# Performance work log

Measured on AMD Instinct MI355X. Metric: run time of the kernel, lower is better.

Reference implementation:

```python
import jax, jax.numpy as jnp
import numpy as np

B, S, E, NH = 2, 1024, 2048, 16
DH = E // NH
EPS = 1e-6

def setup_inputs() -> dict:
    key = jax.random.key(0)
    ks = jax.random.split(key, 6)
    q = jax.random.normal(ks[0], (B, S, E), dtype=jnp.float32)
    k = jax.random.normal(ks[1], (B, S, E), dtype=jnp.float32)
    v = jax.random.normal(ks[2], (B, S, E), dtype=jnp.float32)
    Wi = jax.random.normal(ks[3], (3 * E, NH), dtype=jnp.float32) * 0.02
    bi = jax.random.normal(ks[4], (NH,), dtype=jnp.float32) * 0.1
    Wf = jax.random.normal(ks[5], (3 * E, NH), dtype=jnp.float32) * 0.02
    bf = jnp.linspace(3.0, 6.0, NH, dtype=jnp.float32)  # bias_linspace_initializer(3,6)
    ln_scale = jnp.ones((E,), dtype=jnp.float32)
    return {"q": q, "k": k, "v": v, "Wi": Wi, "bi": bi, "Wf": Wf, "bf": bf, "ln_scale": ln_scale}

def _mlstm_forward(q, k, v, Wi, bi, Wf, bf, ln_scale):
    b, s, e = q.shape
    nh = Wi.shape[1]
    dh = e // nh
    x = jnp.concatenate([q, k, v], axis=-1)                     # (B,S,3E)
    ig = (x @ Wi + bi).transpose(0, 2, 1)[..., None]            # (B,NH,S,1)
    fg = (x @ Wf + bf).transpose(0, 2, 1)[..., None]            # (B,NH,S,1)
    split = lambda t: t.reshape(b, s, nh, dh).transpose(0, 2, 1, 3)
    qh, kh, vh = split(q), split(k), split(v)                   # (B,NH,S,DH)
    # parallel_stabilized_simple backend
    log_f = jax.nn.log_sigmoid(fg)                              # (B,NH,S,1)
    log_f_cum = jnp.concatenate(
        [jnp.zeros((b, nh, 1, 1), q.dtype), jnp.cumsum(log_f, axis=2)], axis=2
    )                                                           # (B,NH,S+1,1)
    # D[i,j] = cumsum[i] - cumsum[j] on causal part
    fg_mat = log_f_cum - jnp.transpose(log_f_cum, (0, 1, 3, 2)) # (B,NH,S+1,S+1)
    ltr = jnp.tril(jnp.ones((s, s), dtype=bool))
    log_fg = jnp.where(ltr, fg_mat[:, :, 1:, 1:], -jnp.inf)     # (B,NH,S,S)
    log_D = log_fg + jnp.transpose(ig, (0, 1, 3, 2))            # + i_j per column
    max_log_D = jnp.max(log_D, axis=-1, keepdims=True)          # (B,NH,S,1)
    D = jnp.exp(log_D - max_log_D)
    qk = jnp.einsum('bhsd,bhtd->bhst', qh, kh) / jnp.sqrt(jnp.asarray(dh, q.dtype))
    C = qk * D                                                  # (B,NH,S,S)
    normalizer = jnp.maximum(jnp.abs(C.sum(-1, keepdims=True)), jnp.exp(-max_log_D))
    Cn = C / (normalizer + EPS)
    h = jnp.einsum('bhst,bhtd->bhsd', Cn, vh)                   # (B,NH,S,DH)
    # MultiHeadLayerNorm: normalize over DH per head, scale (no bias)
    mu = h.mean(-1, keepdims=True)
    var = ((h - mu) ** 2).mean(-1, keepdims=True)
    hn = (h - mu) * jax.lax.rsqrt(var + EPS)
    hn = hn * ln_scale.reshape(1, nh, 1, dh)
    return hn.transpose(0, 2, 1, 3).reshape(b, s, e)            # (B,S,E)

def reference(q, k, v, Wi, bi, Wf, bf, ln_scale):
    return _mlstm_forward(q, k, v, Wi, bi, Wf, bf, ln_scale)
```

## Files before the change

### kernel.cpp

```cpp
#include <hip/hip_runtime.h>
#include <hip/hip_bf16.h>

#define B_   2
#define S_   1024
#define E_   2048
#define NH_  16
#define DH_  128
#define EPS_ 1e-6f

using half8   = __attribute__((ext_vector_type(8))) _Float16;
using floatx4 = __attribute__((ext_vector_type(4))) float;

__device__ __forceinline__ half8 cvt8h(const float* __restrict__ p) {
    float4 a = *(const float4*)p;
    float4 b = *(const float4*)(p + 4);
    half8 r;
    r[0] = (_Float16)a.x; r[1] = (_Float16)a.y;
    r[2] = (_Float16)a.z; r[3] = (_Float16)a.w;
    r[4] = (_Float16)b.x; r[5] = (_Float16)b.y;
    r[6] = (_Float16)b.z; r[7] = (_Float16)b.w;
    return r;
}

__global__ __launch_bounds__(256, 4) void gates_kernel(
    const float* __restrict__ q, const float* __restrict__ k,
    const float* __restrict__ v, const float* __restrict__ Wi,
    const float* __restrict__ Wf, float* __restrict__ pre_i,
    float* __restrict__ pre_f, _Float16* __restrict__ qhg,
    _Float16* __restrict__ khg, _Float16* __restrict__ vtg)
{
    __shared__ __attribute__((aligned(16))) _Float16 xs[32 * 264];
    __shared__ __attribute__((aligned(16))) _Float16 wt[32 * 264];

    const int t    = threadIdx.x;
    const int w    = t >> 6, lane = t & 63, quad = lane >> 4, l15 = lane & 15;
    const int mw   = w & 1, nw = w >> 1;
    const int m0   = blockIdx.x * 32;
    const int by   = blockIdx.y;
    const int kbase = by * 768;
    const int bblk = m0 >> 10;
    const int s0   = m0 & 1023;

    floatx4 acc = {0.f, 0.f, 0.f, 0.f};

    for (int c = 0; c < 3; ++c) {
        __syncthreads();
        const int e0   = kbase + c * 256;
        const int tsel = e0 >> 11;
        const int el0  = e0 & 2047;
        const float* xb = (tsel == 0) ? q : (tsel == 1) ? k : v;
        _Float16* fout = (tsel == 0) ? qhg : khg;
        #pragma unroll
        for (int i = 0; i < 4; ++i) {
            int g = t + i * 256;
            int row = g >> 5, grp = g & 31;
            half8 s8 = cvt8h(xb + (size_t)(m0 + row) * E_ + el0 + grp * 8);
            *(half8*)(&xs[row * 264 + grp * 8]) = s8;
            if (tsel < 2) {
                int el = el0 + grp * 8;
                int h  = el >> 7, d = el & 127;
                *(half8*)(fout + ((size_t)(bblk * NH_ + h) * S_ + s0 + row) * DH_ + d) = s8;
            }
        }
        {
            const int kk = t;
            const float* wiRow = Wi + (size_t)(e0 + kk) * NH_;
            const float* wfRow = Wf + (size_t)(e0 + kk) * NH_;
            float wif[16], wff[16];
            #pragma unroll
            for (int i4 = 0; i4 < 4; ++i4) {
                float4 a = *(const float4*)(wiRow + i4 * 4);
                wif[i4*4+0]=a.x; wif[i4*4+1]=a.y; wif[i4*4+2]=a.z; wif[i4*4+3]=a.w;
                float4 b = *(const float4*)(wfRow + i4 * 4);
                wff[i4*4+0]=b.x; wff[i4*4+1]=b.y; wff[i4*4+2]=b.z; wff[i4*4+3]=b.w;
            }
            #pragma unroll
            for (int hh = 0; hh < 16; ++hh) wt[hh * 264 + kk]        = (_Float16)wif[hh];
            #pragma unroll
            for (int hh = 0; hh < 16; ++hh) wt[(16 + hh) * 264 + kk] = (_Float16)wff[hh];
        }
        __syncthreads();
        if (tsel == 2) {
            const int col = t;
            const int el  = el0 + col;
            const int h   = el >> 7, d = el & 127;
            _Float16 tmp[32];
            #pragma unroll
            for (int r = 0; r < 32; ++r) tmp[r] = xs[r * 264 + col];
            const size_t vo = ((size_t)(bblk * NH_ + h) * DH_ + d) * S_ + s0;
            #pragma unroll
            for (int i = 0; i < 4; ++i)
                *(half8*)(vtg + vo + i * 8) = *(half8*)(&tmp[i * 8]);
        }
        #pragma unroll
        for (int ks = 0; ks < 8; ++ks) {
            half8 af = *(const half8*)(&xs[(mw * 16 + l15) * 264 + ks * 32 + quad * 8]);
            half8 bw = *(const half8*)(&wt[(nw * 16 + l15) * 264 + ks * 32 + quad * 8]);
            acc = __builtin_amdgcn_mfma_f32_16x16x32_f16(af, bw, acc, 0, 0, 0);
        }
    }
    #pragma unroll
    for (int reg = 0; reg < 4; ++reg) {
        int m   = m0 + mw * 16 + quad * 4 + reg;
        int b   = m >> 10, s = m & 1023;
        int col = nw * 16 + l15;
        float vacc = acc[reg];
        if (col < 16)
            pre_i[((size_t)(by * 32 + b * NH_ + col)) * S_ + s] = vacc;
        else
            pre_f[((size_t)(by * 32 + b * NH_ + col - 16)) * S_ + s] = vacc;
    }
}

__global__ __launch_bounds__(256, 2) void attn_kernel(
    const _Float16* __restrict__ qh, const _Float16* __restrict__ kh,
    const _Float16* __restrict__ vtg, const float* __restrict__ pre_i,
    const float* __restrict__ pre_f, const float* __restrict__ bi,
    const float* __restrict__ bfb, const float* __restrict__ lnsc,
    float* __restrict__ out)
{
    __shared__ __attribute__((aligned(16))) _Float16 Ks[64 * 136];
    __shared__ __attribute__((aligned(16))) _Float16 Vt[128 * 72];
    __shared__ __attribute__((aligned(16))) _Float16 Pb[64 * 72];
    __shared__ __attribute__((aligned(16))) float ajAll[1024];
    __shared__ float cq64[64], nf64[64];
    __shared__ float wsum[4], wmax[4];
    __shared__ float lpart[2][2][32];
    __shared__ float spart[2][2][32];
    __shared__ float qpart[2][2][32];

    const int t    = threadIdx.x;
    const int w    = t >> 6, lane = t & 63, quad = lane >> 4, l15 = lane & 15;
    const int mw   = w & 1, nw = w >> 1;
    const int L    = blockIdx.x;
    int qi, bh;
    if (L < 256) { qi = L >> 5;                bh = L & 31; }
    else         { qi = 15 - ((L - 256) >> 5); bh = (L - 256) & 31; }
    const int b    = bh >> 4, h = bh & 15;
    const int q0   = qi * 64;
    const int krow = t >> 2, kd0 = (t & 3) * 32;
    const int vd   = t >> 1, vj0 = (t & 1) * 32;

    {
        const int e4 = t * 4;
        const float bih = bi[h], bfh = bfb[h];
        float ig4[4] = {bih, bih, bih, bih};
        float x4[4]  = {bfh, bfh, bfh, bfh};
        #pragma unroll
        for (int y = 0; y < 8; ++y) {
            float4 pi = *(const float4*)(pre_i + ((size_t)(y * 32 + bh)) * S_ + e4);
            float4 pf = *(const float4*)(pre_f + ((size_t)(y * 32 + bh)) * S_ + e4);
            ig4[0] += pi.x; ig4[1] += pi.y; ig4[2] += pi.z; ig4[3] += pi.w;
            x4[0]  += pf.x; x4[1]  += pf.y; x4[2]  += pf.z; x4[3]  += pf.w;
        }
        float lf[4], ls = 0.f;
        #pragma unroll
        for (int e = 0; e < 4; ++e) {
            float x = x4[e];
            float l = (x >= 0.f) ? -log1pf(__expf(-x)) : (x - log1pf(__expf(x)));
            ls += l; lf[e] = ls;
        }
        float sc = ls;
        #pragma unroll
        for (int off = 1; off < 64; off <<= 1) {
            float o = __shfl_up(sc, off);
            if (lane >= off) sc += o;
        }
        float sexcl = sc - ls;
        if (lane == 63) wsum[w] = sc;
        __syncthreads();
        float Foff = 0.f;
        for (int i = 0; i < w; ++i) Foff += wsum[i];
        float Fbase = Foff + sexcl;
        float av[4], lm[4], am = -3.0e38f;
        #pragma unroll
        for (int e = 0; e < 4; ++e) {
            float F = Fbase + lf[e];
            float a = ig4[e] - F;
            av[e] = a; am = fmaxf(am, a); lm[e] = am;
        }
        *(float4*)(&ajAll[e4]) = *(float4*)av;
        float msc = am;
        #pragma unroll
        for (int off = 1; off < 64; off <<= 1) {
            float o = __shfl_up(msc, off);
            if (lane >= off) msc = fmaxf(msc, o);
        }
        float mprev = __shfl_up(msc, 1);
        float mexcl = (lane == 0) ? -3.0e38f : mprev;
        if (lane == 63) wmax[w] = msc;
        __syncthreads();
        float Moff = -3.0e38f;
        for (int i = 0; i < w; ++i) Moff = fmaxf(Moff, wmax[i]);
        float Mbase = fmaxf(Moff, mexcl);
        #pragma unroll
        for (int e = 0; e < 4; ++e) {
            int s = e4 + e;
            if (s >= q0 && s < q0 + 64) {
                float M = fmaxf(Mbase, lm[e]);
                float F = Fbase + lf[e];
                cq64[s - q0] = -M;
                nf64[s - q0] = expf(fminf(-(F + M), 80.f));
            }
        }
    }
    __syncthreads();

    float ci_r[2][4], nfv_r[2][4];
    #pragma unroll
    for (int s = 0; s < 2; ++s)
        #pragma unroll
        for (int reg = 0; reg < 4; ++reg) {
            int rr = mw * 32 + s * 16 + quad * 4 + reg;
            ci_r[s][reg]  = cq64[rr];
            nfv_r[s][reg] = nf64[rr];
        }
    half8 aq[2][4];
    #pragma unroll
    for (int s = 0; s < 2; ++s) {
        const _Float16* qrow = qh + ((size_t)bh * S_ + q0 + mw * 32 + s * 16 + l15) * DH_;
        #pragma unroll
        for (int ks = 0; ks < 4; ++ks)
            aq[s][ks] = *(const half8*)(qrow + ks * 32 + quad * 8);
    }

    half8 kreg[4], vreg[4];
    {
        const _Float16* kp = kh + ((size_t)bh * S_ + krow) * DH_ + kd0;
        const _Float16* vp = vtg + ((size_t)bh * DH_ + vd) * S_ + vj0;
        #pragma unroll
        for (int i = 0; i < 4; ++i) { kreg[i] = *(const half8*)(kp + i * 8);
                                      vreg[i] = *(const half8*)(vp + i * 8); }
    }
    #pragma unroll
    for (int i = 0; i < 4; ++i) {
        *(half8*)(&Ks[krow * 136 + kd0 + i * 8]) = kreg[i];
        *(half8*)(&Vt[vd * 72 + vj0 + i * 8])    = vreg[i];
    }
    __syncthreads();

    floatx4 acc_h[2][4];
    #pragma unroll
    for (int s = 0; s < 2; ++s)
        #pragma unroll
        for (int i = 0; i < 4; ++i) acc_h[s][i] = (floatx4){0.f, 0.f, 0.f, 0.f};
    float lrun[2][4] = {{0.f, 0.f, 0.f, 0.f}, {0.f, 0.f, 0.f, 0.f}};
    const float rscale = 0.08838834764831845f;

    for (int kt = 0; kt <= qi; ++kt) {
        if (kt < qi) {
            const int j0n = (kt + 1) * 64;
            const _Float16* kp = kh + ((size_t)bh * S_ + j0n + krow) * DH_ + kd0;
            const _Float16* vp = vtg + ((size_t)bh * DH_ + vd) * S_ + j0n + vj0;
            #pragma unroll
            for (int i = 0; i < 4; ++i) { kreg[i] = *(const half8*)(kp + i * 8);
                                          vreg[i] = *(const half8*)(vp + i * 8); }
        }

        const bool diag = (kt == qi);
        floatx4 sacc[2][2];
        #pragma unroll
        for (int s = 0; s < 2; ++s)
            #pragma unroll
            for (int n = 0; n < 2; ++n) sacc[s][n] = (floatx4){0.f, 0.f, 0.f, 0.f};
        if (!(diag && mw == 0 && nw == 1)) {
            __builtin_amdgcn_s_setprio(1);
            #pragma unroll
            for (int ks = 0; ks < 4; ++ks) {
                #pragma unroll
                for (int n = 0; n < 2; ++n) {
                    half8 bk = *(const half8*)(&Ks[(nw * 32 + n * 16 + l15) * 136 + ks * 32 + quad * 8]);
                    sacc[0][n] = __builtin_amdgcn_mfma_f32_16x16x32_f16(aq[0][ks], bk, sacc[0][n], 0, 0, 0);
                    sacc[1][n] = __builtin_amdgcn_mfma_f32_16x16x32_f16(aq[1][ks], bk, sacc[1][n], 0, 0, 0);
                }
            }
            __builtin_amdgcn_s_setprio(0);
        }
        #pragma unroll
        for (int n = 0; n < 2; ++n) {
            int jl = nw * 32 + n * 16 + l15;
            float a_j = ajAll[kt * 64 + jl];
            #pragma unroll
            for (int s = 0; s < 2; ++s) {
                #pragma unroll
                for (int reg = 0; reg < 4; ++reg) {
                    int rloc = mw * 32 + s * 16 + quad * 4 + reg;
                    float p = 0.f;
                    if (!diag || (jl <= rloc))
                        p = sacc[s][n][reg] * rscale * __expf(fminf(ci_r[s][reg] + a_j, 0.f));
                    lrun[s][reg] += p;
                    Pb[rloc * 72 + jl] = (_Float16)p;
                }
            }
        }
        __syncthreads();

        if (kt < qi) {
            #pragma unroll
            for (int i = 0; i < 4; ++i)
                *(half8*)(&Ks[krow * 136 + kd0 + i * 8]) = kreg[i];
        }
        __builtin_amdgcn_s_setprio(1);
        #pragma unroll
        for (int ks2 = 0; ks2 < 2; ++ks2) {
            half8 ap0 = *(const half8*)(&Pb[(mw * 32 + l15) * 72 + ks2 * 32 + quad * 8]);
            half8 ap1 = *(const half8*)(&Pb[(mw * 32 + 16 + l15) * 72 + ks2 * 32 + quad * 8]);
            #pragma unroll
            for (int n = 0; n < 4; ++n) {
                half8 bv = *(const half8*)(&Vt[(nw * 64 + n * 16 + l15) * 72 + ks2 * 32 + quad * 8]);
                acc_h[0][n] = __builtin_amdgcn_mfma_f32_16x16x32_f16(ap0, bv, acc_h[0][n], 0, 0, 0);
                acc_h[1][n] = __builtin_amdgcn_mfma_f32_16x16x32_f16(ap1, bv, acc_h[1][n], 0, 0, 0);
            }
        }
        __builtin_amdgcn_s_setprio(0);
        __syncthreads();

        if (kt < qi) {
            #pragma unroll
            for (int i = 0; i < 4; ++i)
                *(half8*)(&Vt[vd * 72 + vj0 + i * 8]) = vreg[i];
        }
    }

    #pragma unroll
    for (int s = 0; s < 2; ++s)
        #pragma unroll
        for (int reg = 0; reg < 4; ++reg) {
            float l = lrun[s][reg];
            l += __shfl_xor(l, 1); l += __shfl_xor(l, 2);
            l += __shfl_xor(l, 4); l += __shfl_xor(l, 8);
            if (l15 == 0) lpart[nw][mw][s * 16 + quad * 4 + reg] = l;
        }
    __syncthreads();
    float inv_r[2][4];
    #pragma unroll
    for (int s = 0; s < 2; ++s)
        #pragma unroll
        for (int reg = 0; reg < 4; ++reg) {
            int rr = s * 16 + quad * 4 + reg;
            float ltot = lpart[0][mw][rr] + lpart[1][mw][rr];
            inv_r[s][reg] = 1.f / (fmaxf(fabsf(ltot), nfv_r[s][reg]) + EPS_);
        }
    #pragma unroll
    for (int s = 0; s < 2; ++s)
        #pragma unroll
        for (int reg = 0; reg < 4; ++reg) {
            float sum = 0.f, sq = 0.f;
            #pragma unroll
            for (int n = 0; n < 4; ++n) {
                float x = acc_h[s][n][reg] * inv_r[s][reg];
                sum += x; sq += x * x;
            }
            sum += __shfl_xor(sum, 1); sq += __shfl_xor(sq, 1);
            sum += __shfl_xor(sum, 2); sq += __shfl_xor(sq, 2);
            sum += __shfl_xor(sum, 4); sq += __shfl_xor(sq, 4);
            sum += __shfl_xor(sum, 8); sq += __shfl_xor(sq, 8);
            if (l15 == 0) {
                spart[nw][mw][s * 16 + quad * 4 + reg] = sum;
                qpart[nw][mw][s * 16 + quad * 4 + reg] = sq;
            }
        }
    __syncthreads();
    #pragma unroll
    for (int s = 0; s < 2; ++s)
        #pragma unroll
        for (int reg = 0; reg < 4; ++reg) {
            int rr   = s * 16 + quad * 4 + reg;
            float sum = spart[0][mw][rr] + spart[1][mw][rr];
            float sq  = qpart[0][mw][rr] + qpart[1][mw][rr];
            float mean = sum * (1.f / 128.f);
            float var  = fmaxf(sq * (1.f / 128.f) - mean * mean, 0.f);
            float rstd = rsqrtf(var + EPS_);
            int rl = q0 + mw * 32 + rr;
            size_t orow = ((size_t)b * S_ + rl) * E_ + h * DH_;
            #pragma unroll
            for (int n = 0; n < 4; ++n) {
                int d = nw * 64 + n * 16 + l15;
                out[orow + d] = (acc_h[s][n][reg] * inv_r[s][reg] - mean) * rstd * lnsc[h * DH_ + d];
            }
        }
}

extern "C" void kernel_launch(void* const* d_in, const int* in_sizes, int n_in,
                              void* d_out, int out_size, void* d_ws, size_t ws_size,
                              hipStream_t stream)
{
    const float* q    = (const float*)d_in[0];
    const float* k    = (const float*)d_in[1];
    const float* v    = (const float*)d_in[2];
    const float* Wi   = (const float*)d_in[3];
    const float* bi   = (const float*)d_in[4];
    const float* Wf   = (const float*)d_in[5];
    const float* bfb  = (const float*)d_in[6];
    const float* lnsc = (const float*)d_in[7];
    float* out        = (float*)d_out;

    const int NS  = B_ * NH_ * S_;
    float* pre_i = (float*)d_ws;
    float* pre_f = pre_i + 8 * NS;
    _Float16* qh  = (_Float16*)(pre_f + 8 * NS);
    _Float16* kh  = qh + (size_t)32 * S_ * DH_;
    _Float16* vtg = kh + (size_t)32 * S_ * DH_;

    gates_kernel<<<dim3(64, 8), 256, 0, stream>>>(q, k, v, Wi, Wf, pre_i, pre_f,
                                                  qh, kh, vtg);
    attn_kernel<<<dim3(512), 256, 0, stream>>>(qh, kh, vtg, pre_i, pre_f,
                                               bi, bfb, lnsc, out);
}
```

Before: 146.5 us.

## Load K and V MFMA fragments directly from global into registers, double-buffer P

Drops the shared-memory staging of K and V tiles. Each wave now loads its MFMA B-operand fragments straight from global memory into registers and prefetches the next tile after using the current one. The P tile is double-buffered in shared memory, which removes one of the two block barriers per iteration. The trade-off is that waves sharing the same nw each fetch the same K/V data separately, raising global/L2 traffic, and more registers are held for the prefetched fragments.

```diff
diff --git a/kernel.cpp b/kernel.cpp
--- a/kernel.cpp
+++ b/kernel.cpp
@@ -119,9 +119,7 @@
     const float* __restrict__ bfb, const float* __restrict__ lnsc,
     float* __restrict__ out)
 {
-    __shared__ __attribute__((aligned(16))) _Float16 Ks[64 * 136];
-    __shared__ __attribute__((aligned(16))) _Float16 Vt[128 * 72];
-    __shared__ __attribute__((aligned(16))) _Float16 Pb[64 * 72];
+    __shared__ __attribute__((aligned(16))) _Float16 Pb[2][64 * 72];
     __shared__ __attribute__((aligned(16))) float ajAll[1024];
     __shared__ float cq64[64], nf64[64];
     __shared__ float wsum[4], wmax[4];
@@ -138,8 +136,29 @@
     else         { qi = 15 - ((L - 256) >> 5); bh = (L - 256) & 31; }
     const int b    = bh >> 4, h = bh & 15;
     const int q0   = qi * 64;
-    const int krow = t >> 2, kd0 = (t & 3) * 32;
-    const int vd   = t >> 1, vj0 = (t & 1) * 32;
+
+    const _Float16* kfb = kh  + ((size_t)bh * S_  + nw * 32 + l15) * DH_ + quad * 8;
+    const _Float16* vfb = vtg + ((size_t)bh * DH_ + nw * 64 + l15) * S_ + quad * 8;
+
+    half8 kcur[4][2], vcur[2][4];
+    #pragma unroll
+    for (int n = 0; n < 2; ++n)
+        #pragma unroll
+        for (int ks = 0; ks < 4; ++ks)
+            kcur[ks][n] = *(const half8*)(kfb + n * 16 * DH_ + ks * 32);
+    #pragma unroll
+    for (int n = 0; n < 4; ++n)
+        #pragma unroll
+        for (int ks2 = 0; ks2 < 2; ++ks2)
+            vcur[ks2][n] = *(const half8*)(vfb + n * 16 * S_ + ks2 * 32);
+    half8 aq[2][4];
+    #pragma unroll
+    for (int s = 0; s < 2; ++s) {
+        const _Float16* qrow = qh + ((size_t)bh * S_ + q0 + mw * 32 + s * 16 + l15) * DH_;
+        #pragma unroll
+        for (int ks = 0; ks < 4; ++ks)
+            aq[s][ks] = *(const half8*)(qrow + ks * 32 + quad * 8);
+    }
 
     {
         const int e4 = t * 4;
@@ -215,29 +234,6 @@
             ci_r[s][reg]  = cq64[rr];
             nfv_r[s][reg] = nf64[rr];
         }
-    half8 aq[2][4];
-    #pragma unroll
-    for (int s = 0; s < 2; ++s) {
-        const _Float16* qrow = qh + ((size_t)bh * S_ + q0 + mw * 32 + s * 16 + l15) * DH_;
-        #pragma unroll
-        for (int ks = 0; ks < 4; ++ks)
-            aq[s][ks] = *(const half8*)(qrow + ks * 32 + quad * 8);
-    }
-
-    half8 kreg[4], vreg[4];
-    {
-        const _Float16* kp = kh + ((size_t)bh * S_ + krow) * DH_ + kd0;
-        const _Float16* vp = vtg + ((size_t)bh * DH_ + vd) * S_ + vj0;
-        #pragma unroll
-        for (int i = 0; i < 4; ++i) { kreg[i] = *(const half8*)(kp + i * 8);
-                                      vreg[i] = *(const half8*)(vp + i * 8); }
-    }
-    #pragma unroll
-    for (int i = 0; i < 4; ++i) {
-        *(half8*)(&Ks[krow * 136 + kd0 + i * 8]) = kreg[i];
-        *(half8*)(&Vt[vd * 72 + vj0 + i * 8])    = vreg[i];
-    }
-    __syncthreads();
 
     floatx4 acc_h[2][4];
     #pragma unroll
@@ -248,15 +244,6 @@
     const float rscale = 0.08838834764831845f;
 
     for (int kt = 0; kt <= qi; ++kt) {
-        if (kt < qi) {
-            const int j0n = (kt + 1) * 64;
-            const _Float16* kp = kh + ((size_t)bh * S_ + j0n + krow) * DH_ + kd0;
-            const _Float16* vp = vtg + ((size_t)bh * DH_ + vd) * S_ + j0n + vj0;
-            #pragma unroll
-            for (int i = 0; i < 4; ++i) { kreg[i] = *(const half8*)(kp + i * 8);
-                                          vreg[i] = *(const half8*)(vp + i * 8); }
-        }
-
         const bool diag = (kt == qi);
         floatx4 sacc[2][2];
         #pragma unroll
@@ -269,13 +256,21 @@
             for (int ks = 0; ks < 4; ++ks) {
                 #pragma unroll
                 for (int n = 0; n < 2; ++n) {
-                    half8 bk = *(const half8*)(&Ks[(nw * 32 + n * 16 + l15) * 136 + ks * 32 + quad * 8]);
-                    sacc[0][n] = __builtin_amdgcn_mfma_f32_16x16x32_f16(aq[0][ks], bk, sacc[0][n], 0, 0, 0);
-                    sacc[1][n] = __builtin_amdgcn_mfma_f32_16x16x32_f16(aq[1][ks], bk, sacc[1][n], 0, 0, 0);
+                    sacc[0][n] = __builtin_amdgcn_mfma_f32_16x16x32_f16(aq[0][ks], kcur[ks][n], sacc[0][n], 0, 0, 0);
+                    sacc[1][n] = __builtin_amdgcn_mfma_f32_16x16x32_f16(aq[1][ks], kcur[ks][n], sacc[1][n], 0, 0, 0);
                 }
             }
             __builtin_amdgcn_s_setprio(0);
         }
+        if (kt < qi) {
+            const _Float16* kp = kfb + (size_t)(kt + 1) * 64 * DH_;
+            #pragma unroll
+            for (int n = 0; n < 2; ++n)
+                #pragma unroll
+                for (int ks = 0; ks < 4; ++ks)
+                    kcur[ks][n] = *(const half8*)(kp + n * 16 * DH_ + ks * 32);
+        }
+        _Float16* pb = &Pb[kt & 1][0];
         #pragma unroll
         for (int n = 0; n < 2; ++n) {
             int jl = nw * 32 + n * 16 + l15;
@@ -289,36 +284,31 @@
                     if (!diag || (jl <= rloc))
                         p = sacc[s][n][reg] * rscale * __expf(fminf(ci_r[s][reg] + a_j, 0.f));
                     lrun[s][reg] += p;
-                    Pb[rloc * 72 + jl] = (_Float16)p;
+                    pb[rloc * 72 + jl] = (_Float16)p;
                 }
             }
         }
         __syncthreads();
 
+        __builtin_amdgcn_s_setprio(1);
+        #pragma unroll
+        for (int ks2 = 0; ks2 < 2; ++ks2) {
+            half8 ap0 = *(const half8*)(&pb[(mw * 32 + l15) * 72 + ks2 * 32 + quad * 8]);
+            half8 ap1 = *(const half8*)(&pb[(mw * 32 + 16 + l15) * 72 + ks2 * 32 + quad * 8]);
+            #pragma unroll
+            for (int n = 0; n < 4; ++n) {
+                acc_h[0][n] = __builtin_amdgcn_mfma_f32_16x16x32_f16(ap0, vcur[ks2][n], acc_h[0][n], 0, 0, 0);
+                acc_h[1][n] = __builtin_amdgcn_mfma_f32_16x16x32_f16(ap1, vcur[ks2][n], acc_h[1][n], 0, 0, 0);
+            }
+        }
+        __builtin_amdgcn_s_setprio(0);
         if (kt < qi) {
-            #pragma unroll
-            for (int i = 0; i < 4; ++i)
-                *(half8*)(&Ks[krow * 136 + kd0 + i * 8]) = kreg[i];
-        }
-        __builtin_amdgcn_s_setprio(1);
-        #pragma unroll
-        for (int ks2 = 0; ks2 < 2; ++ks2) {
-            half8 ap0 = *(const half8*)(&Pb[(mw * 32 + l15) * 72 + ks2 * 32 + quad * 8]);
-            half8 ap1 = *(const half8*)(&Pb[(mw * 32 + 16 + l15) * 72 + ks2 * 32 + quad * 8]);
-            #pragma unroll
-            for (int n = 0; n < 4; ++n) {
-                half8 bv = *(const half8*)(&Vt[(nw * 64 + n * 16 + l15) * 72 + ks2 * 32 + quad * 8]);
-                acc_h[0][n] = __builtin_amdgcn_mfma_f32_16x16x32_f16(ap0, bv, acc_h[0][n], 0, 0, 0);
-                acc_h[1][n] = __builtin_amdgcn_mfma_f32_16x16x32_f16(ap1, bv, acc_h[1][n], 0, 0, 0);
-            }
-        }
-        __builtin_amdgcn_s_setprio(0);
-        __syncthreads();
-
-        if (kt < qi) {
-            #pragma unroll
-            for (int i = 0; i < 4; ++i)
-                *(half8*)(&Vt[vd * 72 + vj0 + i * 8]) = vreg[i];
+            const _Float16* vp = vfb + (size_t)(kt + 1) * 64;
+            #pragma unroll
+            for (int n = 0; n < 4; ++n)
+                #pragma unroll
+                for (int ks2 = 0; ks2 < 2; ++ks2)
+                    vcur[ks2][n] = *(const half8*)(vp + n * 16 * S_ + ks2 * 32);
         }
     }
 
```

Measured after the change: 152.8 us. 1.04x slower.
